# Kernel tuning notes

Measured on AMD Instinct MI355X. Metric: run time of the kernel, lower is better.

## Reference

```python
import jax, jax.numpy as jnp
import numpy as np

DIM = 512
HEADS = 8
HEAD_DIM = DIM // HEADS
SCALE = HEAD_DIM ** -0.5
LN_EPS = 1e-5


def _layernorm(t, g, b):
    mu = jnp.mean(t, axis=-1, keepdims=True)
    var = jnp.mean(jnp.square(t - mu), axis=-1, keepdims=True)
    return (t - mu) * jax.lax.rsqrt(var + LN_EPS) * g + b


def setup_inputs() -> dict:
    key = jax.random.key(0)
    ks = jax.random.split(key, 8)
    B, C, H, W = 2, DIM, 48, 48
    s = 1.0 / np.sqrt(DIM)
    return {
        "x": jax.random.normal(ks[0], (B, C, H, W), jnp.float32),
        "y": jax.random.normal(ks[1], (B, C, H, W), jnp.float32),
        # linear weights stored [in, out]
        "k_w": jax.random.uniform(ks[2], (DIM, DIM), jnp.float32, -s, s),
        "k_b": jax.random.uniform(ks[3], (DIM,), jnp.float32, -s, s),
        "qv_w": jax.random.uniform(ks[4], (DIM, 2 * DIM), jnp.float32, -s, s),
        "qv_b": jax.random.uniform(ks[5], (2 * DIM,), jnp.float32, -s, s),
        "lnx_g": jnp.ones((DIM,), jnp.float32),
        "lnx_b": jnp.zeros((DIM,), jnp.float32),
        "lny_g": jnp.ones((DIM,), jnp.float32),
        "lny_b": jnp.zeros((DIM,), jnp.float32),
    }


def _split_qv(t, qv_w, qv_b):
    B, N, C = t.shape
    qv = (t @ qv_w + qv_b).reshape(B, N, 2, HEADS, HEAD_DIM)
    qv = jnp.transpose(qv, (2, 0, 3, 1, 4))  # [2, B, h, N, d]
    return qv[0], qv[1]


def _heads(t):
    B, N, C = t.shape
    return jnp.transpose(t.reshape(B, N, HEADS, HEAD_DIM), (0, 2, 1, 3))  # [B,h,N,d]


def reference(x, y, k_w, k_b, qv_w, qv_b, lnx_g, lnx_b, lny_g, lny_b):
    B, C = x.shape[0], x.shape[1]
    xf = _layernorm(jnp.transpose(x.reshape(B, C, -1), (0, 2, 1)), lnx_g, lnx_b)  # [B,N,C]
    yf = _layernorm(jnp.transpose(y.reshape(B, C, -1), (0, 2, 1)), lny_g, lny_b)
    N = xf.shape[1]

    y_q, y_v = _split_qv(yf, qv_w, qv_b)
    x_q, x_v = _split_qv(xf, qv_w, qv_b)
    y_k = _heads(yf @ k_w + k_b)
    x_k = _heads(xf @ k_w + k_b)

    # branch 1: softmax(x_q y_k^T) x_v  -> standard [B,N,C]
    a1 = jax.nn.softmax(jnp.einsum('bhnd,bhmd->bhnm', x_q, y_k) * SCALE, axis=-1)
    xo = jnp.einsum('bhnm,bhmd->bhnd', a1, x_v)
    xo = jnp.transpose(xo, (0, 2, 1, 3)).reshape(B, N, C)

    # branch 2: faithful reproduction of torch quirk (x_k kept a leading 1-dim,
    # so the output [1,B,h,N,d].transpose(1,2).reshape(B,N,C) scrambles layout)
    a2 = jax.nn.softmax(jnp.einsum('bhnd,bhmd->bhnm', y_q, x_k) * SCALE, axis=-1)
    yo = jnp.einsum('bhnm,bhmd->bhnd', a2, y_v)  # [B,h,N,d]
    yo = jnp.transpose(yo[None], (0, 2, 1, 3, 4)).reshape(B, N, C)

    return jnp.concatenate([xo, yo], axis=0)  # [2B, N, C]
```

## Files before the change

kernel.cpp:

```cpp
#include <hip/hip_runtime.h>

#define DIM 512
#define NTOK 2304
#define HEADS 8
#define HD 64
#define LN_EPS 1e-5f
#define BNC 2359296
#define QSC 0.18033688011112042f

typedef __attribute__((ext_vector_type(8))) short short8;
typedef __attribute__((ext_vector_type(4))) short sh4;
typedef __attribute__((ext_vector_type(4))) float f32x4;

__device__ __forceinline__ short f2bf(float f) {
    union { float f; unsigned u; } x; x.f = f;
    unsigned r = (x.u + 0x7fffu + ((x.u >> 16) & 1u)) >> 16;
    return (short)(r & 0xffffu);
}
__device__ __forceinline__ unsigned fbits(float f) {
    union { float f; unsigned u; } x; x.f = f; return x.u;
}
__device__ __forceinline__ void gl2lds(const short* g, short* l) {
    __builtin_amdgcn_global_load_lds(
        (const __attribute__((address_space(1))) unsigned int*)g,
        (__attribute__((address_space(3))) unsigned int*)l, 16, 0, 0);
}

__global__ void k_pre(const float* __restrict__ x, const float* __restrict__ y,
                      const float* __restrict__ qv_w, const float* __restrict__ k_w,
                      const float* __restrict__ qv_b, const float* __restrict__ k_b,
                      const float* __restrict__ gx, const float* __restrict__ bx,
                      const float* __restrict__ gy, const float* __restrict__ by,
                      short* __restrict__ T, short* __restrict__ Wt,
                      float* __restrict__ bias) {
    __shared__ __align__(16) float tile[64][65];
    __shared__ float pS[4][64], pQ[4][64];
    __shared__ float muL[64], rsL[64];
    int bkid = blockIdx.x, tid = threadIdx.x;
    if (bkid < 1152) {
        int nt = bkid % 36, ct = (bkid / 36) % 8, sb = bkid / 288;
        int s = sb >> 1, b = sb & 1;
        int n0 = nt * 64, c0 = ct * 64;
        const float* src = (s ? y : x) + (size_t)b * DIM * NTOK;
        int nl = tid & 63, part = tid >> 6;
        {
            const float* p = src + n0 + nl;
            float sum = 0.f, sq = 0.f;
            for (int c = part * 128; c < part * 128 + 128; c++) {
                float v = p[(size_t)c * NTOK];
                sum += v; sq += v * v;
            }
            pS[part][nl] = sum; pQ[part][nl] = sq;
        }
        __syncthreads();
        if (tid < 64) {
            float ts = pS[0][tid] + pS[1][tid] + pS[2][tid] + pS[3][tid];
            float tq = pQ[0][tid] + pQ[1][tid] + pQ[2][tid] + pQ[3][tid];
            float m = ts * (1.0f / DIM);
            float var = tq * (1.0f / DIM) - m * m;
            muL[tid] = m;
            rsL[tid] = rsqrtf(var + LN_EPS);
        }
        for (int slot = tid; slot < 1024; slot += 256) {
            int r = slot >> 4, q = slot & 15;
            const float* p = src + (size_t)(c0 + r) * NTOK + n0 + q * 4;
            float4 v = *(const float4*)p;
            tile[r][q*4+0] = v.x; tile[r][q*4+1] = v.y;
            tile[r][q*4+2] = v.z; tile[r][q*4+3] = v.w;
        }
        __syncthreads();
        const float* g  = s ? gy : gx;
        const float* be = s ? by : bx;
        int nr = tid >> 2, cg = tid & 3;
        float m = muL[nr], r_ = rsL[nr];
        short8 o0, o1;
        for (int i = 0; i < 8; i++) {
            int c = c0 + cg * 16 + i;
            o0[i] = f2bf((tile[cg*16+i][nr] - m) * r_ * g[c] + be[c]);
        }
        for (int i = 0; i < 8; i++) {
            int c = c0 + cg * 16 + 8 + i;
            o1[i] = f2bf((tile[cg*16+8+i][nr] - m) * r_ * g[c] + be[c]);
        }
        short* dst = T + ((size_t)sb * NTOK + n0 + nr) * DIM + c0 + cg * 16;
        *(short8*)dst = o0;
        *(short8*)(dst + 8) = o1;
        return;
    }
    int idx = bkid - 1152;
    int jt = idx % 24, ct = idx / 24;
    int j0 = jt * 64, c0 = ct * 64;
    if (ct == 0 && tid < 64) {
        int j = j0 + tid;
        bias[j] = (j < 1024) ? qv_b[j] : k_b[j - 1024];
    }
    for (int slot = tid; slot < 1024; slot += 256) {
        int r = slot >> 4, q = slot & 15;
        int c = c0 + r;
        float4 v;
        if (j0 < 1024) v = *(const float4*)(qv_w + (size_t)c * 1024 + j0 + q * 4);
        else           v = *(const float4*)(k_w  + (size_t)c * 512  + (j0 - 1024) + q * 4);
        tile[r][q*4+0] = v.x; tile[r][q*4+1] = v.y;
        tile[r][q*4+2] = v.z; tile[r][q*4+3] = v.w;
    }
    __syncthreads();
    int jr = tid >> 2, cg = tid & 3;
    short8 o0, o1;
    for (int i = 0; i < 8; i++) o0[i] = f2bf(tile[cg*16+i][jr]);
    for (int i = 0; i < 8; i++) o1[i] = f2bf(tile[cg*16+8+i][jr]);
    short* dst = Wt + (size_t)(j0 + jr) * DIM + c0 + cg * 16;
    *(short8*)dst = o0;
    *(short8*)(dst + 8) = o1;
}

__global__ void __launch_bounds__(256)
k_gemm(const short* __restrict__ T, const short* __restrict__ Wt,
       const float* __restrict__ bias, short* __restrict__ QVK,
       short* __restrict__ VT) {
    __shared__ __align__(16) short Abuf[2][128 * 64];
    __shared__ __align__(16) short Bbuf[2][128 * 64];
    int n0 = blockIdx.x * 128, j0 = blockIdx.y * 128, sb = blockIdx.z;
    int tid = threadIdx.x;
    int w = tid >> 6, l = tid & 63;
    int wr = w >> 1, wc = w & 1;
    int lrow = l & 15, quad = l >> 4;
    int r_in = (l >> 3) & 7, cc = l & 7;
    int ch = cc ^ r_in;
    int sw0 = (quad ^ (lrow & 7)) * 8;
    const short* Ab = T + (size_t)sb * NTOK * DIM;
    f32x4 acc[4][4] = {};

    #pragma unroll
    for (int inst = 0; inst < 4; inst++) {
        int R = w * 32 + inst * 8 + r_in;
        gl2lds(Ab + (size_t)(n0 + R) * 512 + 0 * 64 + ch * 8, &Abuf[0][(w * 32 + inst * 8) * 64]);
        gl2lds(Wt + (size_t)(j0 + R) * 512 + 0 * 64 + ch * 8, &Bbuf[0][(w * 32 + inst * 8) * 64]);
    }
    int cur = 0;
    for (int kk = 0; kk < 8; kk++) {
        __syncthreads();
        if (kk + 1 < 8) {
            #pragma unroll
            for (int inst = 0; inst < 4; inst++) {
                int R = w * 32 + inst * 8 + r_in;
                gl2lds(Ab + (size_t)(n0 + R) * 512 + (kk + 1) * 64 + ch * 8,
                       &Abuf[cur ^ 1][(w * 32 + inst * 8) * 64]);
                gl2lds(Wt + (size_t)(j0 + R) * 512 + (kk + 1) * 64 + ch * 8,
                       &Bbuf[cur ^ 1][(w * 32 + inst * 8) * 64]);
            }
        }
        #pragma unroll
        for (int c2 = 0; c2 < 2; c2++) {
            int off = c2 ? (sw0 ^ 32) : sw0;
            short8 af[4], bf[4];
            #pragma unroll
            for (int i = 0; i < 4; i++)
                af[i] = *(const short8*)&Abuf[cur][(wr*64 + i*16 + lrow) * 64 + off];
            #pragma unroll
            for (int j = 0; j < 4; j++)
                bf[j] = *(const short8*)&Bbuf[cur][(wc*64 + j*16 + lrow) * 64 + off];
            #pragma unroll
            for (int i = 0; i < 4; i++)
                #pragma unroll
                for (int j = 0; j < 4; j++)
                    acc[i][j] = __builtin_amdgcn_mfma_f32_16x16x32_bf16(bf[j], af[i], acc[i][j], 0, 0, 0);
        }
        cur ^= 1;
    }
    if (j0 >= 512 && j0 < 1024) {
        __syncthreads();
        short* sm = &Abuf[0][0];
        #pragma unroll
        for (int i = 0; i < 4; i++)
            #pragma unroll
            for (int j = 0; j < 4; j++) {
                int jb = wc * 64 + j * 16 + quad * 4;
                int nloc = wr * 64 + i * 16 + lrow;
                float4 bv4 = *(const float4*)&bias[j0 + jb];
                float bvs[4] = {bv4.x, bv4.y, bv4.z, bv4.w};
                #pragma unroll
                for (int reg = 0; reg < 4; reg++) {
                    int jloc = jb + reg;
                    sm[jloc * 128 + (((nloc >> 3) ^ (jloc & 15)) * 8) + (nloc & 7)]
                        = f2bf(acc[i][j][reg] + bvs[reg]);
                }
            }
        __syncthreads();
        for (int slot = tid; slot < 2048; slot += 256) {
            int row = slot >> 4, seg = slot & 15;
            short8 v = *(const short8*)&sm[row * 128 + ((seg ^ (row & 15)) * 8)];
            *(short8*)(VT + ((size_t)sb * 512 + (j0 - 512) + row) * NTOK + n0 + seg * 8) = v;
        }
    } else {
        #pragma unroll
        for (int i = 0; i < 4; i++) {
            int n = n0 + wr * 64 + i * 16 + lrow;
            #pragma unroll
            for (int j = 0; j < 4; j++) {
                int jjb = j0 + wc * 64 + j * 16 + quad * 4;
                float4 bv4 = *(const float4*)&bias[jjb];
                float bvs[4] = {bv4.x, bv4.y, bv4.z, bv4.w};
                float sc = (jjb < 512) ? QSC : 1.0f;
                sh4 pk;
                #pragma unroll
                for (int reg = 0; reg < 4; reg++)
                    pk[reg] = f2bf((acc[i][j][reg] + bvs[reg]) * sc);
                *(sh4*)&QVK[((size_t)sb * NTOK + n) * 1536 + jjb] = pk;
            }
        }
    }
}

__global__ void __launch_bounds__(256)
k_attn(const short* __restrict__ QVK, const short* __restrict__ VT,
       float* __restrict__ out, float* __restrict__ O1,
       float* __restrict__ l0, float* __restrict__ l1) {
    __shared__ __align__(16) short Kbuf[2][64 * 64];
    __shared__ __align__(16) short Vbuf[2][64 * 64];
    __shared__ __align__(16) short Qs[64 * 64];
    int id = blockIdx.x;
    int half = id / 1152;
    int rid = id % 1152;
    int xcd = rid & 7, rem = rid >> 3;
    int qt = rem % 36, yhi = rem / 36;
    int yb = yhi * 8 + xcd;
    int br = yb >> 4;
    int b  = (yb >> 3) & 1;
    int h  = yb & 7;
    int tid = threadIdx.x;
    int w = tid >> 6, l = tid & 63;
    int lrow = l & 15, quad = l >> 4;
    int r_in = (l >> 3) & 7, cc = l & 7;
    int ch = cc ^ r_in;
    int sw0 = (quad ^ (lrow & 7)) * 8;
    int n0 = qt * 64;
    int m_base = half * 1152;
    const short* Qg = QVK + ((size_t)(br * 2 + b) * NTOK) * 1536 + h * 64;
    const short* Kg = QVK + ((size_t)((1 - br) * 2 + b) * NTOK) * 1536 + 1024 + h * 64;
    const short* Vg = VT + ((size_t)(br * 2 + b) * 512 + h * 64) * NTOK;

    for (int inst = 0; inst < 2; inst++) {
        int R = w * 16 + inst * 8 + r_in;
        gl2lds(Qg + (size_t)(n0 + R) * 1536 + ch * 8, &Qs[(w * 16 + inst * 8) * 64]);
    }

    const short* KnA = Kg + (size_t)(m_base + w * 16 + r_in) * 1536 + ch * 8;
    const short* KnB = Kg + (size_t)(m_base + w * 16 + 8 + r_in) * 1536 + ch * 8;
    const short* VnA = Vg + (size_t)(w * 16 + r_in) * NTOK + m_base + ch * 8;
    const short* VnB = Vg + (size_t)(w * 16 + 8 + r_in) * NTOK + m_base + ch * 8;
    int lds_off = l * 8;

    short8 ka = *(const short8*)(KnA);
    short8 kb = *(const short8*)(KnB);
    short8 va = *(const short8*)(VnA);
    short8 vb = *(const short8*)(VnB);
    KnA += (size_t)64 * 1536; KnB += (size_t)64 * 1536;
    VnA += 64; VnB += 64;

    __syncthreads();
    short8 bq0 = *(const short8*)&Qs[(w * 16 + lrow) * 64 + sw0];
    short8 bq1 = *(const short8*)&Qs[(w * 16 + lrow) * 64 + (sw0 ^ 32)];
    short* Pw = &Qs[w * 16 * 64];

    *(short8*)&Kbuf[0][(w * 16)     * 64 + lds_off] = ka;
    *(short8*)&Kbuf[0][(w * 16 + 8) * 64 + lds_off] = kb;
    *(short8*)&Vbuf[0][(w * 16)     * 64 + lds_off] = va;
    *(short8*)&Vbuf[0][(w * 16 + 8) * 64 + lds_off] = vb;
    ka = *(const short8*)(KnA);
    kb = *(const short8*)(KnB);
    va = *(const short8*)(VnA);
    vb = *(const short8*)(VnB);
    KnA += (size_t)64 * 1536; KnB += (size_t)64 * 1536;
    VnA += 64; VnB += 64;

    short8 ones;
    for (int i = 0; i < 8; i++) ones[i] = (short)0x3F80;

    f32x4 Oacc[4] = {};
    f32x4 lacc = {};
    int cur = 0;

    for (int mt = 0; mt < 18; mt++) {
        __syncthreads();
        const short* Ks = Kbuf[cur];
        const short* Vs = Vbuf[cur];

        for (int sub = 0; sub < 4; sub++) {
            short8 ak0 = *(const short8*)&Ks[(sub * 16 + lrow) * 64 + sw0];
            short8 ak1 = *(const short8*)&Ks[(sub * 16 + lrow) * 64 + (sw0 ^ 32)];
            f32x4 a = {};
            a = __builtin_amdgcn_mfma_f32_16x16x32_bf16(ak0, bq0, a, 0, 0, 0);
            a = __builtin_amdgcn_mfma_f32_16x16x32_bf16(ak1, bq1, a, 0, 0, 0);
            float p0 = __builtin_amdgcn_exp2f(a[0]), p1 = __builtin_amdgcn_exp2f(a[1]);
            float p2 = __builtin_amdgcn_exp2f(a[2]), p3 = __builtin_amdgcn_exp2f(a[3]);
            uint2 pk;
            pk.x = __builtin_amdgcn_perm(fbits(p1), fbits(p0), 0x07060302u);
            pk.y = __builtin_amdgcn_perm(fbits(p3), fbits(p2), 0x07060302u);
            *(uint2*)&Pw[lrow * 64 + (((2 * sub + (quad >> 1)) ^ (lrow & 7)) * 8) + (quad & 1) * 4] = pk;
        }

        short8 ap0 = *(const short8*)&Pw[lrow * 64 + sw0];
        short8 ap1 = *(const short8*)&Pw[lrow * 64 + (sw0 ^ 32)];
        lacc = __builtin_amdgcn_mfma_f32_16x16x32_bf16(ones, ap0, lacc, 0, 0, 0);
        lacc = __builtin_amdgcn_mfma_f32_16x16x32_bf16(ones, ap1, lacc, 0, 0, 0);
        for (int ddt = 0; ddt < 4; ddt++) {
            short8 av0 = *(const short8*)&Vs[(ddt * 16 + lrow) * 64 + sw0];
            short8 av1 = *(const short8*)&Vs[(ddt * 16 + lrow) * 64 + (sw0 ^ 32)];
            Oacc[ddt] = __builtin_amdgcn_mfma_f32_16x16x32_bf16(av0, ap0, Oacc[ddt], 0, 0, 0);
            Oacc[ddt] = __builtin_amdgcn_mfma_f32_16x16x32_bf16(av1, ap1, Oacc[ddt], 0, 0, 0);
        }

        if (mt + 1 < 18) {
            *(short8*)&Kbuf[cur ^ 1][(w * 16)     * 64 + lds_off] = ka;
            *(short8*)&Kbuf[cur ^ 1][(w * 16 + 8) * 64 + lds_off] = kb;
            *(short8*)&Vbuf[cur ^ 1][(w * 16)     * 64 + lds_off] = va;
            *(short8*)&Vbuf[cur ^ 1][(w * 16 + 8) * 64 + lds_off] = vb;
        }
        if (mt + 2 < 18) {
            ka = *(const short8*)(KnA);
            kb = *(const short8*)(KnB);
            va = *(const short8*)(VnA);
            vb = *(const short8*)(VnB);
        }
        KnA += (size_t)64 * 1536; KnB += (size_t)64 * 1536;
        VnA += 64; VnB += 64;
        cur ^= 1;
    }

    int n = n0 + w * 16 + lrow;
    if (quad == 0) (half ? l1 : l0)[yb * NTOK + n] = lacc[0];
    for (int ddt = 0; ddt < 4; ddt++) {
        float4 o;
        o.x = Oacc[ddt][0];
        o.y = Oacc[ddt][1];
        o.z = Oacc[ddt][2];
        o.w = Oacc[ddt][3];
        if (half == 0) {
            if (br == 0)
                *(float4*)&out[((size_t)b * NTOK + n) * 512 + h * 64 + ddt * 16 + quad * 4] = o;
            else
                *(float4*)&out[(size_t)BNC + ((size_t)(h * 2 + b) * NTOK + n) * 64 + ddt * 16 + quad * 4] = o;
        } else {
            *(float4*)&O1[((size_t)yb * NTOK + n) * 64 + ddt * 16 + quad * 4] = o;
        }
    }
}

__global__ void __launch_bounds__(256)
k_norm(float* __restrict__ out, const float* __restrict__ O1,
       const float* __restrict__ l0, const float* __restrict__ l1) {
    int i = blockIdx.x * 256 + threadIdx.x;
    int o = i * 4;
    int yb, n, d;
    if (o < BNC) {
        int b = o / (NTOK * 512);
        int r = o % (NTOK * 512);
        n = r >> 9;
        int c = r & 511;
        d = c & 63;
        yb = b * 8 + (c >> 6);
    } else {
        int o2 = o - BNC;
        int hb = o2 / (NTOK * 64);
        n = (o2 >> 6) % NTOK;
        d = o2 & 63;
        yb = 16 + (hb & 1) * 8 + (hb >> 1);
    }
    int li = yb * NTOK + n;
    float linv = 1.f / (l0[li] + l1[li]);
    float4 a = *(const float4*)&out[o];
    float4 q = *(const float4*)&O1[(size_t)li * 64 + d];
    a.x = (a.x + q.x) * linv;
    a.y = (a.y + q.y) * linv;
    a.z = (a.z + q.z) * linv;
    a.w = (a.w + q.w) * linv;
    *(float4*)&out[o] = a;
}

extern "C" void kernel_launch(void* const* d_in, const int* in_sizes, int n_in,
                              void* d_out, int out_size, void* d_ws, size_t ws_size,
                              hipStream_t stream) {
    const float* x     = (const float*)d_in[0];
    const float* y     = (const float*)d_in[1];
    const float* k_w   = (const float*)d_in[2];
    const float* k_b   = (const float*)d_in[3];
    const float* qv_w  = (const float*)d_in[4];
    const float* qv_b  = (const float*)d_in[5];
    const float* lnx_g = (const float*)d_in[6];
    const float* lnx_b = (const float*)d_in[7];
    const float* lny_g = (const float*)d_in[8];
    const float* lny_b = (const float*)d_in[9];
    float* out = (float*)d_out;

    char* ws = (char*)d_ws;
    float* bias = (float*)ws;
    short* T    = (short*)(ws + 6144);
    short* Wt   = T + 4718592;
    short* QVK  = Wt + 786432;
    short* VT   = QVK + 14155776;
    float* O1   = (float*)(ws + 48764928);
    float* l0   = (float*)(ws + 67639296);
    float* l1   = (float*)(ws + 67934208);

    k_pre  <<<1344, 256, 0, stream>>>(x, y, qv_w, k_w, qv_b, k_b,
                                      lnx_g, lnx_b, lny_g, lny_b, T, Wt, bias);
    k_gemm <<<dim3(18, 12, 4), 256, 0, stream>>>(T, Wt, bias, QVK, VT);
    k_attn <<<2304, 256, 0, stream>>>(QVK, VT, out, O1, l0, l1);
    k_norm <<<4608, 256, 0, stream>>>(out, O1, l0, l1);
}
```

Baseline: 203.9 us.

## Generalize attention KV split count and raise MFMA wave priority

The attention kernel now splits the key/value sequence into a configurable number of chunks (4 when the workspace is large enough, otherwise 2), and writes partial outputs and row sums into generalized buffers. The norm kernel then sums all the partials. This raises the number of blocks so more can run at once. It also wraps the MFMA sections in s_setprio to favour matrix-issue waves. The cost is more partial-output memory traffic in the reduction kernel, and the extra splits depend on the workspace size.

```diff
diff --git a/kernel.cpp b/kernel.cpp
--- a/kernel.cpp
+++ b/kernel.cpp
@@ -213,8 +213,8 @@
 
 __global__ void __launch_bounds__(256)
 k_attn(const short* __restrict__ QVK, const short* __restrict__ VT,
-       float* __restrict__ out, float* __restrict__ O1,
-       float* __restrict__ l0, float* __restrict__ l1) {
+       float* __restrict__ out, float* __restrict__ Opart,
+       float* __restrict__ lbuf, int ntiles) {
     __shared__ __align__(16) short Kbuf[2][64 * 64];
     __shared__ __align__(16) short Vbuf[2][64 * 64];
     __shared__ __align__(16) short Qs[64 * 64];
@@ -234,7 +234,7 @@
     int ch = cc ^ r_in;
     int sw0 = (quad ^ (lrow & 7)) * 8;
     int n0 = qt * 64;
-    int m_base = half * 1152;
+    int m_base = half * ntiles * 64;
     const short* Qg = QVK + ((size_t)(br * 2 + b) * NTOK) * 1536 + h * 64;
     const short* Kg = QVK + ((size_t)((1 - br) * 2 + b) * NTOK) * 1536 + 1024 + h * 64;
     const short* Vg = VT + ((size_t)(br * 2 + b) * 512 + h * 64) * NTOK;
@@ -280,7 +280,7 @@
     f32x4 lacc = {};
     int cur = 0;
 
-    for (int mt = 0; mt < 18; mt++) {
+    for (int mt = 0; mt < ntiles; mt++) {
         __syncthreads();
         const short* Ks = Kbuf[cur];
         const short* Vs = Vbuf[cur];
@@ -289,8 +289,10 @@
             short8 ak0 = *(const short8*)&Ks[(sub * 16 + lrow) * 64 + sw0];
             short8 ak1 = *(const short8*)&Ks[(sub * 16 + lrow) * 64 + (sw0 ^ 32)];
             f32x4 a = {};
+            __builtin_amdgcn_s_setprio(1);
             a = __builtin_amdgcn_mfma_f32_16x16x32_bf16(ak0, bq0, a, 0, 0, 0);
             a = __builtin_amdgcn_mfma_f32_16x16x32_bf16(ak1, bq1, a, 0, 0, 0);
+            __builtin_amdgcn_s_setprio(0);
             float p0 = __builtin_amdgcn_exp2f(a[0]), p1 = __builtin_amdgcn_exp2f(a[1]);
             float p2 = __builtin_amdgcn_exp2f(a[2]), p3 = __builtin_amdgcn_exp2f(a[3]);
             uint2 pk;
@@ -301,6 +303,7 @@
 
         short8 ap0 = *(const short8*)&Pw[lrow * 64 + sw0];
         short8 ap1 = *(const short8*)&Pw[lrow * 64 + (sw0 ^ 32)];
+        __builtin_amdgcn_s_setprio(1);
         lacc = __builtin_amdgcn_mfma_f32_16x16x32_bf16(ones, ap0, lacc, 0, 0, 0);
         lacc = __builtin_amdgcn_mfma_f32_16x16x32_bf16(ones, ap1, lacc, 0, 0, 0);
         for (int ddt = 0; ddt < 4; ddt++) {
@@ -309,14 +312,15 @@
             Oacc[ddt] = __builtin_amdgcn_mfma_f32_16x16x32_bf16(av0, ap0, Oacc[ddt], 0, 0, 0);
             Oacc[ddt] = __builtin_amdgcn_mfma_f32_16x16x32_bf16(av1, ap1, Oacc[ddt], 0, 0, 0);
         }
-
-        if (mt + 1 < 18) {
+        __builtin_amdgcn_s_setprio(0);
+
+        if (mt + 1 < ntiles) {
             *(short8*)&Kbuf[cur ^ 1][(w * 16)     * 64 + lds_off] = ka;
             *(short8*)&Kbuf[cur ^ 1][(w * 16 + 8) * 64 + lds_off] = kb;
             *(short8*)&Vbuf[cur ^ 1][(w * 16)     * 64 + lds_off] = va;
             *(short8*)&Vbuf[cur ^ 1][(w * 16 + 8) * 64 + lds_off] = vb;
         }
-        if (mt + 2 < 18) {
+        if (mt + 2 < ntiles) {
             ka = *(const short8*)(KnA);
             kb = *(const short8*)(KnB);
             va = *(const short8*)(VnA);
@@ -328,7 +332,7 @@
     }
 
     int n = n0 + w * 16 + lrow;
-    if (quad == 0) (half ? l1 : l0)[yb * NTOK + n] = lacc[0];
+    if (quad == 0) lbuf[half * (32 * NTOK) + yb * NTOK + n] = lacc[0];
     for (int ddt = 0; ddt < 4; ddt++) {
         float4 o;
         o.x = Oacc[ddt][0];
@@ -341,14 +345,15 @@
             else
                 *(float4*)&out[(size_t)BNC + ((size_t)(h * 2 + b) * NTOK + n) * 64 + ddt * 16 + quad * 4] = o;
         } else {
-            *(float4*)&O1[((size_t)yb * NTOK + n) * 64 + ddt * 16 + quad * 4] = o;
+            *(float4*)&Opart[(size_t)(half - 1) * 4718592 +
+                             ((size_t)yb * NTOK + n) * 64 + ddt * 16 + quad * 4] = o;
         }
     }
 }
 
 __global__ void __launch_bounds__(256)
-k_norm(float* __restrict__ out, const float* __restrict__ O1,
-       const float* __restrict__ l0, const float* __restrict__ l1) {
+k_norm(float* __restrict__ out, const float* __restrict__ Opart,
+       const float* __restrict__ lbuf, int ns) {
     int i = blockIdx.x * 256 + threadIdx.x;
     int o = i * 4;
     int yb, n, d;
@@ -367,13 +372,15 @@
         yb = 16 + (hb & 1) * 8 + (hb >> 1);
     }
     int li = yb * NTOK + n;
-    float linv = 1.f / (l0[li] + l1[li]);
+    float lsum = 0.f;
+    for (int k = 0; k < ns; k++) lsum += lbuf[k * (32 * NTOK) + li];
+    float linv = 1.f / lsum;
     float4 a = *(const float4*)&out[o];
-    float4 q = *(const float4*)&O1[(size_t)li * 64 + d];
-    a.x = (a.x + q.x) * linv;
-    a.y = (a.y + q.y) * linv;
-    a.z = (a.z + q.z) * linv;
-    a.w = (a.w + q.w) * linv;
+    for (int k = 1; k < ns; k++) {
+        float4 q = *(const float4*)&Opart[(size_t)(k - 1) * 4718592 + (size_t)li * 64 + d];
+        a.x += q.x; a.y += q.y; a.z += q.z; a.w += q.w;
+    }
+    a.x *= linv; a.y *= linv; a.z *= linv; a.w *= linv;
     *(float4*)&out[o] = a;
 }
 
@@ -398,13 +405,16 @@
     short* Wt   = T + 4718592;
     short* QVK  = Wt + 786432;
     short* VT   = QVK + 14155776;
-    float* O1   = (float*)(ws + 48764928);
-    float* l0   = (float*)(ws + 67639296);
-    float* l1   = (float*)(ws + 67934208);
+    float* lbuf = (float*)(ws + 48764928);
+    float* Opart= (float*)(ws + 49944576);
+
+    int ns = (ws_size >= 49944576ull + 3ull * 18874368ull) ? 4
+           : (ws_size >= 49944576ull + 1ull * 18874368ull) ? 2 : 2;
+    int ntiles = 36 / ns;
 
     k_pre  <<<1344, 256, 0, stream>>>(x, y, qv_w, k_w, qv_b, k_b,
                                       lnx_g, lnx_b, lny_g, lny_b, T, Wt, bias);
     k_gemm <<<dim3(18, 12, 4), 256, 0, stream>>>(T, Wt, bias, QVK, VT);
-    k_attn <<<2304, 256, 0, stream>>>(QVK, VT, out, O1, l0, l1);
-    k_norm <<<4608, 256, 0, stream>>>(out, O1, l0, l1);
-}
+    k_attn <<<1152 * ns, 256, 0, stream>>>(QVK, VT, out, Opart, lbuf, ntiles);
+    k_norm <<<4608, 256, 0, stream>>>(out, Opart, lbuf, ns);
+}
```

Result: slower. 210.2 us (+3.1%).
